# Performance work log

Hardware: AMD Instinct MI355X
Metric: run time of the kernel (lower is better)

The kernel has to match this reference:

```python
import jax, jax.numpy as jnp
import numpy as np
from jax import lax

SIGMA = 1.0
ALPHA = 1.0
BETA = 1.0
TRUNCATE = 4.0  # scipy.ndimage default


def _gauss_kernel(sigma):
    radius = int(TRUNCATE * sigma + 0.5)  # scipy radius rule -> 4 for sigma=1
    x = np.arange(-radius, radius + 1, dtype=np.float64)
    k = np.exp(-0.5 * (x / sigma) ** 2)
    k = (k / k.sum()).astype(np.float32)
    return k

_KERNEL = _gauss_kernel(SIGMA)


def _blur_axis(img, k, axis):
    # scipy mode='reflect' == jnp.pad mode='symmetric' (edge repeated)
    r = len(k) // 2
    pad = [(0, 0)] * img.ndim
    pad[axis] = (r, r)
    xp = jnp.pad(img, pad, mode='symmetric')
    n = img.shape[axis]
    out = k[0] * lax.slice_in_dim(xp, 0, n, axis=axis)
    for i in range(1, len(k)):
        out = out + k[i] * lax.slice_in_dim(xp, i, i + n, axis=axis)
    return out


def gaussian_blur(img):
    # scalar sigma in scipy blurs along EVERY axis, including batch & channel
    k = jnp.asarray(_KERNEL, dtype=img.dtype)
    for ax in range(img.ndim):
        img = _blur_axis(img, k, ax)
    return img


def decompose(I):
    I_log = jnp.log(I + 1e-6)
    I_smooth = gaussian_blur(I_log)
    R = I_log - I_smooth
    L = I_log - R  # == I_smooth
    return jnp.exp(L), jnp.exp(R)


def setup_inputs() -> dict:
    key = jax.random.key(0)
    k1, k2 = jax.random.split(key)
    shape = (16, 3, 512, 512)
    I_enhanced = jax.random.uniform(k1, shape, dtype=jnp.float32)
    I_gt = jax.random.uniform(k2, shape, dtype=jnp.float32)
    return {"I_enhanced": I_enhanced, "I_gt": I_gt}


def reference(I_enhanced, I_gt):
    L_enh, R_enh = decompose(I_enhanced)
    L_gt, R_gt = decompose(I_gt)
    L_reflectance = jnp.mean((R_enh - R_gt) ** 2)
    L_illumination = jnp.mean((L_enh - L_gt) ** 2)
    return ALPHA * L_reflectance + BETA * L_illumination
```

## Files before the change

### kernel.cpp

```cpp
#include <hip/hip_runtime.h>
#include <hip/hip_fp16.h>
#include <cmath>

#define PLANE (512*512)
#define NPLANES 48
#define NEL (48*PLANE)

struct Taps { float k[9]; };
struct CMat { float w[3][3]; };


#define FOLD(r) ((r) < 0 ? (-1 - (r)) : ((r) > 511 ? (1023 - (r)) : (r)))

__global__ __launch_bounds__(128)
void k_blur_hw(const float* __restrict__ inE, const float* __restrict__ inG,
               uint* __restrict__ wsS, uint* __restrict__ wsI, Taps tp)
{
    const int g  = threadIdx.x;
    const int r0 = blockIdx.x * 16;
    const int z  = blockIdx.y;
    const float* __restrict__ srcE = inE + z * PLANE;
    const float* __restrict__ srcG = inG + z * PLANE;
    const int col   = 4 * g;
    const int tile  = col >> 6;
    const int inner = col & 63;
    const bool edge = (g == 0) || (g == 127);
    const int  eoff = (g == 0) ? 0 : 516;

    __shared__ float buf[2][2][520];

    __half2 kh[9];
#pragma unroll
    for (int t = 0; t < 9; ++t) kh[t] = __float2half2_rn(tp.k[t]);

    __half2 ring[12][4];

    float4 pE[3], pG[3];
#pragma unroll
    for (int s = 0; s < 3; ++s) {
        const int row = FOLD(r0 - 4 + s);
        pE[s] = *(const float4*)(srcE + row * 512 + col);
        pG[s] = *(const float4*)(srcG + row * 512 + col);
    }

#pragma unroll
    for (int jb = 0; jb < 24; jb += 12) {
#pragma unroll
        for (int u = 0; u < 12; ++u) {
            const int j   = jb + u;
            const int par = j & 1;

            float4 oe = pE[0], og = pG[0];
            pE[0] = pE[1]; pE[1] = pE[2];
            pG[0] = pG[1]; pG[1] = pG[2];
            if (j + 3 < 24) {
                const int row = FOLD(r0 - 1 + j);
                pE[2] = *(const float4*)(srcE + row * 512 + col);
                pG[2] = *(const float4*)(srcG + row * 512 + col);
            }

            const float e4 = __logf(oe.x + 1e-6f);
            const float e5 = __logf(oe.y + 1e-6f);
            const float e6 = __logf(oe.z + 1e-6f);
            const float e7 = __logf(oe.w + 1e-6f);
            const float g4 = __logf(og.x + 1e-6f);
            const float g5 = __logf(og.y + 1e-6f);
            const float g6 = __logf(og.z + 1e-6f);
            const float g7 = __logf(og.w + 1e-6f);

            *(float4*)&buf[par][0][4 + col] = make_float4(e4, e5, e6, e7);
            *(float4*)&buf[par][1][4 + col] = make_float4(g4, g5, g6, g7);
            if (edge) {
                *(float4*)&buf[par][0][eoff] = make_float4(e7, e6, e5, e4);
                *(float4*)&buf[par][1][eoff] = make_float4(g7, g6, g5, g4);
            }

            if (j >= 4 && j < 20) {
                const int ri = r0 + j - 4;
                __half2 i0 = __floats2half2_rn(oe.x + 1e-6f, og.x + 1e-6f);
                __half2 i1 = __floats2half2_rn(oe.y + 1e-6f, og.y + 1e-6f);
                __half2 i2 = __floats2half2_rn(oe.z + 1e-6f, og.z + 1e-6f);
                __half2 i3 = __floats2half2_rn(oe.w + 1e-6f, og.w + 1e-6f);
                uint* dp = wsI + (((ri * 8 + tile) * 48) + z) * 64 + inner;
                *(uint4*)dp = make_uint4(*(uint*)&i0, *(uint*)&i1,
                                         *(uint*)&i2, *(uint*)&i3);
            }

            __syncthreads();

            float oE0, oE1, oE2, oE3, oG0, oG1, oG2, oG3;
            {
                float4 lA = *(const float4*)&buf[par][0][col];
                float4 lB = *(const float4*)&buf[par][0][col + 8];
                float wv[12] = {lA.x, lA.y, lA.z, lA.w, e4, e5, e6, e7,
                                lB.x, lB.y, lB.z, lB.w};
                float o0 = 0.f, o1 = 0.f, o2 = 0.f, o3 = 0.f;
#pragma unroll
                for (int t = 0; t < 9; ++t) {
                    const float kt = tp.k[t];
                    o0 += kt * wv[t];
                    o1 += kt * wv[t + 1];
                    o2 += kt * wv[t + 2];
                    o3 += kt * wv[t + 3];
                }
                oE0 = o0; oE1 = o1; oE2 = o2; oE3 = o3;
            }
            {
                float4 lA = *(const float4*)&buf[par][1][col];
                float4 lB = *(const float4*)&buf[par][1][col + 8];
                float wv[12] = {lA.x, lA.y, lA.z, lA.w, g4, g5, g6, g7,
                                lB.x, lB.y, lB.z, lB.w};
                float o0 = 0.f, o1 = 0.f, o2 = 0.f, o3 = 0.f;
#pragma unroll
                for (int t = 0; t < 9; ++t) {
                    const float kt = tp.k[t];
                    o0 += kt * wv[t];
                    o1 += kt * wv[t + 1];
                    o2 += kt * wv[t + 2];
                    o3 += kt * wv[t + 3];
                }
                oG0 = o0; oG1 = o1; oG2 = o2; oG3 = o3;
            }
            ring[u][0] = __floats2half2_rn(oE0, oG0);
            ring[u][1] = __floats2half2_rn(oE1, oG1);
            ring[u][2] = __floats2half2_rn(oE2, oG2);
            ring[u][3] = __floats2half2_rn(oE3, oG3);

            if (j >= 8) {
                __half2 a0 = __float2half2_rn(0.f), a1 = a0, a2 = a0, a3 = a0;
#pragma unroll
                for (int t = 0; t < 9; ++t) {
                    const int sl = (j - 8 + t) % 12;
                    a0 = __hfma2(kh[t], ring[sl][0], a0);
                    a1 = __hfma2(kh[t], ring[sl][1], a1);
                    a2 = __hfma2(kh[t], ring[sl][2], a2);
                    a3 = __hfma2(kh[t], ring[sl][3], a3);
                }
                const int ro = r0 + j - 8;
                uint* dp = wsS + (((ro * 8 + tile) * 48) + z) * 64 + inner;
                *(uint4*)dp = make_uint4(*(uint*)&a0, *(uint*)&a1,
                                         *(uint*)&a2, *(uint*)&a3);
            }
        }
    }
}

__global__ __launch_bounds__(256)
void k_cn_loss(const uint* __restrict__ wsS, const uint* __restrict__ wsI,
               float* __restrict__ out, Taps tp, CMat cm)
{
    const int tid = threadIdx.x;
    const int p   = blockIdx.x * 256 + tid;
    const int w   = p & 511;
    const int h   = p >> 9;
    const int base = ((h * 8 + (w >> 6)) * 48) * 64 + (w & 63);
    const uint* __restrict__ sb = wsS + base;
    const uint* __restrict__ ib = wsI + base;

    __half2 k2[9], cw[3][3];
#pragma unroll
    for (int t = 0; t < 9; ++t) k2[t] = __float2half2_rn(tp.k[t]);
#pragma unroll
    for (int i = 0; i < 3; ++i)
#pragma unroll
        for (int jj = 0; jj < 3; ++jj) cw[i][jj] = __float2half2_rn(cm.w[i][jj]);

    __half2 r[9][3];

#define LOADS(m, u)                                                            \
    u[0] = sb[((m) * 3 + 0) * 64];                                             \
    u[1] = sb[((m) * 3 + 1) * 64];                                             \
    u[2] = sb[((m) * 3 + 2) * 64];

#define CBLUR(u, d)                                                            \
    {                                                                          \
        __half2 v0 = *(__half2*)&u[0];                                         \
        __half2 v1 = *(__half2*)&u[1];                                         \
        __half2 v2 = *(__half2*)&u[2];                                         \
        d[0] = __hfma2(cw[0][0], v0, __hfma2(cw[0][1], v1, __hmul2(cw[0][2], v2))); \
        d[1] = __hfma2(cw[1][0], v0, __hfma2(cw[1][1], v1, __hmul2(cw[1][2], v2))); \
        d[2] = __hfma2(cw[2][0], v0, __hfma2(cw[2][1], v1, __hmul2(cw[2][2], v2))); \
    }

    {
        uint su[3];
#pragma unroll
        for (int m = 0; m < 4; ++m) { LOADS(m, su); CBLUR(su, r[m]); }
    }
    uint nu[3];
    LOADS(4, nu);
    uint iu[3];
    iu[0] = ib[0]; iu[1] = ib[64]; iu[2] = ib[128];

    float acc = 0.f;
#pragma unroll
    for (int n = 0; n < 16; ++n) {
        uint niu[3];
        if (n + 1 < 16) {
#pragma unroll
            for (int c = 0; c < 3; ++c) niu[c] = ib[((n + 1) * 3 + c) * 64];
        }
        const int mnew = n + 4;
        if (mnew < 16) {
            CBLUR(nu, r[mnew % 9]);
            if (mnew + 1 < 16) { LOADS(mnew + 1, nu); }
        }
#pragma unroll
        for (int c = 0; c < 3; ++c) {
            __half2 s2 = __float2half2_rn(0.f);
#pragma unroll
            for (int t = 0; t < 9; ++t) {
                int m = n - 4 + t;
                m = (m < 0) ? (-1 - m) : ((m > 15) ? (31 - m) : m);
                s2 = __hfma2(k2[t], r[m % 9][c], s2);
            }
            const float2 sf  = __half22float2(s2);
            const float2 if2 = __half22float2(*(__half2*)&iu[c]);

            float eE = __expf(-sf.x), eG = __expf(-sf.y);
            float Re = if2.x * eE;
            float Rg = if2.y * eG;
            float Le = __builtin_amdgcn_rcpf(eE);
            float Lg = __builtin_amdgcn_rcpf(eG);
            float dr = Re - Rg, dl = Le - Lg;
            acc += dr * dr + dl * dl;
        }
        if (n + 1 < 16) { iu[0] = niu[0]; iu[1] = niu[1]; iu[2] = niu[2]; }
    }
#undef LOADS
#undef CBLUR

    __shared__ float red[256];
    red[tid] = acc;
    __syncthreads();
#pragma unroll
    for (int s = 128; s > 0; s >>= 1) {
        if (tid < s) red[tid] += red[tid + s];
        __syncthreads();
    }
    if (tid == 0) atomicAdd(out, red[0] * (1.0f / (float)NEL));
}

extern "C" void kernel_launch(void* const* d_in, const int* in_sizes, int n_in,
                              void* d_out, int out_size, void* d_ws, size_t ws_size,
                              hipStream_t stream) {
    const float* Ie = (const float*)d_in[0];
    const float* Ig = (const float*)d_in[1];

    Taps tp;
    {
        double kk[9], s = 0.0;
        for (int i = 0; i < 9; ++i) { double x = (double)(i - 4); kk[i] = exp(-0.5 * x * x); s += kk[i]; }
        for (int i = 0; i < 9; ++i) tp.k[i] = (float)(kk[i] / s);
    }

    CMat cm;
    {
        for (int c = 0; c < 3; ++c) {
            cm.w[c][0] = cm.w[c][1] = cm.w[c][2] = 0.f;
            for (int t = 0; t < 9; ++t) {
                int m = c - 4 + t;
                int mm = ((m % 6) + 6) % 6;
                if (mm > 2) mm = 5 - mm;
                cm.w[c][mm] += tp.k[t];
            }
        }
    }

    uint* wsS = (uint*)d_ws;
    uint* wsI = wsS + (size_t)NEL;

    hipMemsetAsync(d_out, 0, sizeof(float), stream);
    dim3 g1(32, 48);
    k_blur_hw<<<g1, 128, 0, stream>>>(Ie, Ig, wsS, wsI, tp);
    k_cn_loss<<<1024, 256, 0, stream>>>(wsS, wsI, (float*)d_out, tp, cm);
}
```

Baseline: 176.8 us.

## Use single-wavefront blocks with shuffle-based horizontal halo and packed fp16 blur

Restructures the horizontal/vertical blur kernel so that each 64-lane block covers a full 512-wide row, with 8 columns per lane, and neighbouring lanes' values are exchanged with warp shuffles instead of LDS plus __syncthreads. The horizontal pass now runs in packed half2 arithmetic on log values instead of fp32. Row tiles shrink from 16 to 8, so there are more blocks but a larger vertical halo overhead (16 rows loaded for 8 outputs). This aims to remove the barrier and LDS traffic at the cost of more redundant global reads and lower fp16 precision in the horizontal pass.

```diff
diff --git a/kernel.cpp b/kernel.cpp
--- a/kernel.cpp
+++ b/kernel.cpp
@@ -12,135 +12,117 @@
 
 #define FOLD(r) ((r) < 0 ? (-1 - (r)) : ((r) > 511 ? (1023 - (r)) : (r)))
 
-__global__ __launch_bounds__(128)
+__global__ __launch_bounds__(64, 3)
 void k_blur_hw(const float* __restrict__ inE, const float* __restrict__ inG,
                uint* __restrict__ wsS, uint* __restrict__ wsI, Taps tp)
 {
-    const int g  = threadIdx.x;
-    const int r0 = blockIdx.x * 16;
+    const int l  = threadIdx.x;
+    const int r0 = blockIdx.x * 8;
     const int z  = blockIdx.y;
     const float* __restrict__ srcE = inE + z * PLANE;
     const float* __restrict__ srcG = inG + z * PLANE;
-    const int col   = 4 * g;
-    const int tile  = col >> 6;
+    const int col   = 8 * l;
+    const int tile  = l >> 3;
     const int inner = col & 63;
-    const bool edge = (g == 0) || (g == 127);
-    const int  eoff = (g == 0) ? 0 : 516;
-
-    __shared__ float buf[2][2][520];
 
     __half2 kh[9];
 #pragma unroll
     for (int t = 0; t < 9; ++t) kh[t] = __float2half2_rn(tp.k[t]);
 
-    __half2 ring[12][4];
-
-    float4 pE[3], pG[3];
-#pragma unroll
-    for (int s = 0; s < 3; ++s) {
+    __half2 ring[9][8];
+
+    float4 eA[2], eB[2], gA[2], gB[2];
+#pragma unroll
+    for (int s = 0; s < 2; ++s) {
         const int row = FOLD(r0 - 4 + s);
-        pE[s] = *(const float4*)(srcE + row * 512 + col);
-        pG[s] = *(const float4*)(srcG + row * 512 + col);
-    }
-
-#pragma unroll
-    for (int jb = 0; jb < 24; jb += 12) {
-#pragma unroll
-        for (int u = 0; u < 12; ++u) {
-            const int j   = jb + u;
-            const int par = j & 1;
-
-            float4 oe = pE[0], og = pG[0];
-            pE[0] = pE[1]; pE[1] = pE[2];
-            pG[0] = pG[1]; pG[1] = pG[2];
-            if (j + 3 < 24) {
-                const int row = FOLD(r0 - 1 + j);
-                pE[2] = *(const float4*)(srcE + row * 512 + col);
-                pG[2] = *(const float4*)(srcG + row * 512 + col);
-            }
-
-            const float e4 = __logf(oe.x + 1e-6f);
-            const float e5 = __logf(oe.y + 1e-6f);
-            const float e6 = __logf(oe.z + 1e-6f);
-            const float e7 = __logf(oe.w + 1e-6f);
-            const float g4 = __logf(og.x + 1e-6f);
-            const float g5 = __logf(og.y + 1e-6f);
-            const float g6 = __logf(og.z + 1e-6f);
-            const float g7 = __logf(og.w + 1e-6f);
-
-            *(float4*)&buf[par][0][4 + col] = make_float4(e4, e5, e6, e7);
-            *(float4*)&buf[par][1][4 + col] = make_float4(g4, g5, g6, g7);
-            if (edge) {
-                *(float4*)&buf[par][0][eoff] = make_float4(e7, e6, e5, e4);
-                *(float4*)&buf[par][1][eoff] = make_float4(g7, g6, g5, g4);
-            }
-
-            if (j >= 4 && j < 20) {
-                const int ri = r0 + j - 4;
-                __half2 i0 = __floats2half2_rn(oe.x + 1e-6f, og.x + 1e-6f);
-                __half2 i1 = __floats2half2_rn(oe.y + 1e-6f, og.y + 1e-6f);
-                __half2 i2 = __floats2half2_rn(oe.z + 1e-6f, og.z + 1e-6f);
-                __half2 i3 = __floats2half2_rn(oe.w + 1e-6f, og.w + 1e-6f);
-                uint* dp = wsI + (((ri * 8 + tile) * 48) + z) * 64 + inner;
-                *(uint4*)dp = make_uint4(*(uint*)&i0, *(uint*)&i1,
-                                         *(uint*)&i2, *(uint*)&i3);
-            }
-
-            __syncthreads();
-
-            float oE0, oE1, oE2, oE3, oG0, oG1, oG2, oG3;
-            {
-                float4 lA = *(const float4*)&buf[par][0][col];
-                float4 lB = *(const float4*)&buf[par][0][col + 8];
-                float wv[12] = {lA.x, lA.y, lA.z, lA.w, e4, e5, e6, e7,
-                                lB.x, lB.y, lB.z, lB.w};
-                float o0 = 0.f, o1 = 0.f, o2 = 0.f, o3 = 0.f;
-#pragma unroll
-                for (int t = 0; t < 9; ++t) {
-                    const float kt = tp.k[t];
-                    o0 += kt * wv[t];
-                    o1 += kt * wv[t + 1];
-                    o2 += kt * wv[t + 2];
-                    o3 += kt * wv[t + 3];
-                }
-                oE0 = o0; oE1 = o1; oE2 = o2; oE3 = o3;
-            }
-            {
-                float4 lA = *(const float4*)&buf[par][1][col];
-                float4 lB = *(const float4*)&buf[par][1][col + 8];
-                float wv[12] = {lA.x, lA.y, lA.z, lA.w, g4, g5, g6, g7,
-                                lB.x, lB.y, lB.z, lB.w};
-                float o0 = 0.f, o1 = 0.f, o2 = 0.f, o3 = 0.f;
-#pragma unroll
-                for (int t = 0; t < 9; ++t) {
-                    const float kt = tp.k[t];
-                    o0 += kt * wv[t];
-                    o1 += kt * wv[t + 1];
-                    o2 += kt * wv[t + 2];
-                    o3 += kt * wv[t + 3];
-                }
-                oG0 = o0; oG1 = o1; oG2 = o2; oG3 = o3;
-            }
-            ring[u][0] = __floats2half2_rn(oE0, oG0);
-            ring[u][1] = __floats2half2_rn(oE1, oG1);
-            ring[u][2] = __floats2half2_rn(oE2, oG2);
-            ring[u][3] = __floats2half2_rn(oE3, oG3);
-
-            if (j >= 8) {
-                __half2 a0 = __float2half2_rn(0.f), a1 = a0, a2 = a0, a3 = a0;
-#pragma unroll
-                for (int t = 0; t < 9; ++t) {
-                    const int sl = (j - 8 + t) % 12;
-                    a0 = __hfma2(kh[t], ring[sl][0], a0);
-                    a1 = __hfma2(kh[t], ring[sl][1], a1);
-                    a2 = __hfma2(kh[t], ring[sl][2], a2);
-                    a3 = __hfma2(kh[t], ring[sl][3], a3);
-                }
-                const int ro = r0 + j - 8;
-                uint* dp = wsS + (((ro * 8 + tile) * 48) + z) * 64 + inner;
-                *(uint4*)dp = make_uint4(*(uint*)&a0, *(uint*)&a1,
-                                         *(uint*)&a2, *(uint*)&a3);
-            }
+        eA[s] = *(const float4*)(srcE + row * 512 + col);
+        eB[s] = *(const float4*)(srcE + row * 512 + col + 4);
+        gA[s] = *(const float4*)(srcG + row * 512 + col);
+        gB[s] = *(const float4*)(srcG + row * 512 + col + 4);
+    }
+
+#pragma unroll
+    for (int j = 0; j < 16; ++j) {
+        const float4 ea = eA[0], eb = eB[0], ga = gA[0], gb = gB[0];
+        eA[0] = eA[1]; eB[0] = eB[1]; gA[0] = gA[1]; gB[0] = gB[1];
+        if (j + 2 < 16) {
+            const int row = FOLD(r0 - 2 + j);
+            eA[1] = *(const float4*)(srcE + row * 512 + col);
+            eB[1] = *(const float4*)(srcE + row * 512 + col + 4);
+            gA[1] = *(const float4*)(srcG + row * 512 + col);
+            gB[1] = *(const float4*)(srcG + row * 512 + col + 4);
+        }
+
+        if (j >= 4 && j < 12) {
+            const int ri = r0 + j - 4;
+            __half2 i0 = __floats2half2_rn(ea.x + 1e-6f, ga.x + 1e-6f);
+            __half2 i1 = __floats2half2_rn(ea.y + 1e-6f, ga.y + 1e-6f);
+            __half2 i2 = __floats2half2_rn(ea.z + 1e-6f, ga.z + 1e-6f);
+            __half2 i3 = __floats2half2_rn(ea.w + 1e-6f, ga.w + 1e-6f);
+            __half2 i4 = __floats2half2_rn(eb.x + 1e-6f, gb.x + 1e-6f);
+            __half2 i5 = __floats2half2_rn(eb.y + 1e-6f, gb.y + 1e-6f);
+            __half2 i6 = __floats2half2_rn(eb.z + 1e-6f, gb.z + 1e-6f);
+            __half2 i7 = __floats2half2_rn(eb.w + 1e-6f, gb.w + 1e-6f);
+            uint* dp = wsI + (((ri * 8 + tile) * 48) + z) * 64 + inner;
+            *(uint4*)(dp)     = make_uint4(*(uint*)&i0, *(uint*)&i1,
+                                           *(uint*)&i2, *(uint*)&i3);
+            *(uint4*)(dp + 4) = make_uint4(*(uint*)&i4, *(uint*)&i5,
+                                           *(uint*)&i6, *(uint*)&i7);
+        }
+
+        __half2 c[8];
+        c[0] = __floats2half2_rn(__logf(ea.x + 1e-6f), __logf(ga.x + 1e-6f));
+        c[1] = __floats2half2_rn(__logf(ea.y + 1e-6f), __logf(ga.y + 1e-6f));
+        c[2] = __floats2half2_rn(__logf(ea.z + 1e-6f), __logf(ga.z + 1e-6f));
+        c[3] = __floats2half2_rn(__logf(ea.w + 1e-6f), __logf(ga.w + 1e-6f));
+        c[4] = __floats2half2_rn(__logf(eb.x + 1e-6f), __logf(gb.x + 1e-6f));
+        c[5] = __floats2half2_rn(__logf(eb.y + 1e-6f), __logf(gb.y + 1e-6f));
+        c[6] = __floats2half2_rn(__logf(eb.z + 1e-6f), __logf(gb.z + 1e-6f));
+        c[7] = __floats2half2_rn(__logf(eb.w + 1e-6f), __logf(gb.w + 1e-6f));
+
+        __half2 win[16];
+#pragma unroll
+        for (int i = 0; i < 4; ++i) {
+            int v = __shfl_up(*(const int*)&c[4 + i], 1);
+            win[i] = *(__half2*)&v;
+        }
+#pragma unroll
+        for (int i = 0; i < 8; ++i) win[4 + i] = c[i];
+#pragma unroll
+        for (int i = 0; i < 4; ++i) {
+            int v = __shfl_down(*(const int*)&c[i], 1);
+            win[12 + i] = *(__half2*)&v;
+        }
+        if (l == 0) {
+            win[0] = c[3]; win[1] = c[2]; win[2] = c[1]; win[3] = c[0];
+        }
+        if (l == 63) {
+            win[12] = c[7]; win[13] = c[6]; win[14] = c[5]; win[15] = c[4];
+        }
+
+#pragma unroll
+        for (int i = 0; i < 8; ++i) {
+            __half2 a = __hmul2(kh[0], win[i]);
+#pragma unroll
+            for (int t = 1; t < 9; ++t) a = __hfma2(kh[t], win[i + t], a);
+            ring[j % 9][i] = a;
+        }
+
+        if (j >= 8) {
+            __half2 a[8];
+#pragma unroll
+            for (int i = 0; i < 8; ++i) a[i] = __hmul2(kh[0], ring[(j - 8) % 9][i]);
+#pragma unroll
+            for (int t = 1; t < 9; ++t)
+#pragma unroll
+                for (int i = 0; i < 8; ++i)
+                    a[i] = __hfma2(kh[t], ring[(j - 8 + t) % 9][i], a[i]);
+            const int ro = r0 + j - 8;
+            uint* dp = wsS + (((ro * 8 + tile) * 48) + z) * 64 + inner;
+            *(uint4*)(dp)     = make_uint4(*(uint*)&a[0], *(uint*)&a[1],
+                                           *(uint*)&a[2], *(uint*)&a[3]);
+            *(uint4*)(dp + 4) = make_uint4(*(uint*)&a[4], *(uint*)&a[5],
+                                           *(uint*)&a[6], *(uint*)&a[7]);
         }
     }
 }
@@ -271,7 +253,7 @@
     uint* wsI = wsS + (size_t)NEL;
 
     hipMemsetAsync(d_out, 0, sizeof(float), stream);
-    dim3 g1(32, 48);
-    k_blur_hw<<<g1, 128, 0, stream>>>(Ie, Ig, wsS, wsI, tp);
+    dim3 g1(64, 48);
+    k_blur_hw<<<g1, 64, 0, stream>>>(Ie, Ig, wsS, wsI, tp);
     k_cn_loss<<<1024, 256, 0, stream>>>(wsS, wsI, (float*)d_out, tp, cm);
 }
```

New measurement: 197.4 us. 11.7% more time.
